# Kernel tuning notes

Hardware: AMD Instinct MI355X
Metric: run time of the kernel (lower is better)

Reference implementation:

```python
import jax, jax.numpy as jnp
import numpy as np

MOMENTUM = 0.999
TEMP = 0.07
NUM_HARD_NEGS = 16
NUM_CLASSES = 20000


def _normalize(x, axis=-1, eps=1e-12):
    n = jnp.linalg.norm(x, axis=axis, keepdims=True)
    return x / jnp.maximum(n, eps)


def setup_inputs() -> dict:
    key = jax.random.key(0)
    k1, k2, k3, k4, k5 = jax.random.split(key, 5)
    B, K, Dp, De, C = 512, 8, 256, 512, NUM_CLASSES
    return {
        "part_features": jax.random.normal(k1, (B, K, Dp), dtype=jnp.float32),
        "embeddings": jax.random.normal(k2, (B, De), dtype=jnp.float32),
        "sat_emb": jax.random.normal(k3, (B, De), dtype=jnp.float32),
        "part_bank": jax.random.normal(k4, (C, K, Dp), dtype=jnp.float32) * 0.01,
        "embed_bank": jax.random.normal(k5, (C, De), dtype=jnp.float32) * 0.01,
        "labels": jnp.arange(B, dtype=jnp.int64),
    }


def reference(part_features, embeddings, sat_emb, part_bank, embed_bank, labels):
    m = MOMENTUM
    B = embeddings.shape[0]
    C = embed_bank.shape[0]

    # --- EMA scatter update (bank assumed initialized for all classes) ---
    # labels are distinct, so vectorized scatter == sequential python loop.
    new_part_bank = part_bank.at[labels].set(
        m * part_bank[labels] + (1.0 - m) * part_features)
    new_embed_bank = embed_bank.at[labels].set(
        m * embed_bank[labels] + (1.0 - m) * embeddings)

    # Banks are torch buffers updated under no_grad -> stop_gradient.
    eb = jax.lax.stop_gradient(new_embed_bank)

    # --- PrototypeNCE ---
    q = _normalize(embeddings)                      # [B, De]
    protos = _normalize(eb)                         # [C, De]
    sim = (q @ protos.T) / TEMP                     # [B, C]
    pos_sim = jnp.take_along_axis(sim, labels[:, None], axis=1)  # [B, 1]
    class_ids = jnp.arange(C)
    pos_mask = labels[:, None] == class_ids[None, :]
    neg_sim = jnp.where(pos_mask, -1e9, sim)
    hard_negs, _ = jax.lax.top_k(neg_sim, NUM_HARD_NEGS)          # [B, k]
    logits = jnp.concatenate([pos_sim, hard_negs], axis=1)       # [B, 1+k]
    nce_loss = jnp.mean(jax.nn.logsumexp(logits, axis=1) - logits[:, 0])

    # --- Cross-view prototype alignment ---
    p = _normalize(eb[labels])                      # [B, De]
    d = _normalize(embeddings)
    s = _normalize(sat_emb)
    align_loss = 0.5 * (jnp.mean(1.0 - jnp.sum(d * p, axis=-1))
                        + jnp.mean(1.0 - jnp.sum(s * p, axis=-1)))

    return new_part_bank, new_embed_bank, nce_loss, align_loss
```

## Files before the change

kernel.cpp:

```cpp
#include <hip/hip_runtime.h>
#include <math.h>

#define MOM 0.999f
#define ONE_M_MOM 0.001f
#define INV_TEMP (1.0f / 0.07f)
#define C_CLASSES 20000
#define B_SZ 512
#define DE 512
#define PART_ROW 2048
#define PART_BANK_N (C_CLASSES * PART_ROW)
#define EMB_BANK_N (C_CLASSES * DE)
#define NEG_INF (-3.0e38f)
#define NTILE 157
#define NGEMM (4 * NTILE)
#define NCHUNK 2500
#define NPARTB 512

typedef __attribute__((ext_vector_type(8))) short short8;
typedef __attribute__((ext_vector_type(4))) float f32x4;

__device__ inline unsigned short f2bf_rne(float f) {
    unsigned u = __builtin_bit_cast(unsigned, f);
    return (unsigned short)((u + 0x7FFFu + ((u >> 16) & 1u)) >> 16);
}

__device__ inline float bf2f(unsigned short u) {
    return __builtin_bit_cast(float, (unsigned)u << 16);
}

__device__ inline void gload16(const void* g, void* l) {
    __builtin_amdgcn_global_load_lds(
        (const __attribute__((address_space(1))) unsigned int*)g,
        (__attribute__((address_space(3))) unsigned int*)l, 16, 0, 0);
}

__global__ void embed_qnorm(const float* __restrict__ ebank, const float* __restrict__ emb,
                            const int* __restrict__ labels, float* __restrict__ out_eb,
                            unsigned short* __restrict__ Bb, float* __restrict__ inv_norm,
                            unsigned short* __restrict__ Ab, int* __restrict__ counter) {
    int w = threadIdx.x >> 6, l = threadIdx.x & 63;
    int blk = blockIdx.x;
    if (blk == 0 && threadIdx.x == 0) *counter = 0;
    if (blk < 5000) {
        int c = blk * 4 + w;
        int m = -1;
#pragma unroll
        for (int k = 0; k < 8; ++k)
            if (labels[l + k * 64] == c) m = l + k * 64;
#pragma unroll
        for (int off = 32; off; off >>= 1) m = max(m, __shfl_xor(m, off));

        const float4* row = (const float4*)(ebank + ((long)c << 9));
        float4 v0 = row[2 * l], v1 = row[2 * l + 1];
        if (m >= 0) {
            const float4* nr = (const float4*)(emb + ((long)m << 9));
            float4 n0 = nr[2 * l], n1 = nr[2 * l + 1];
            v0.x = MOM * v0.x + ONE_M_MOM * n0.x;
            v0.y = MOM * v0.y + ONE_M_MOM * n0.y;
            v0.z = MOM * v0.z + ONE_M_MOM * n0.z;
            v0.w = MOM * v0.w + ONE_M_MOM * n0.w;
            v1.x = MOM * v1.x + ONE_M_MOM * n1.x;
            v1.y = MOM * v1.y + ONE_M_MOM * n1.y;
            v1.z = MOM * v1.z + ONE_M_MOM * n1.z;
            v1.w = MOM * v1.w + ONE_M_MOM * n1.w;
        }
        float4* orow = (float4*)(out_eb + ((long)c << 9));
        orow[2 * l] = v0; orow[2 * l + 1] = v1;
        float ss = v0.x * v0.x + v0.y * v0.y + v0.z * v0.z + v0.w * v0.w
                 + v1.x * v1.x + v1.y * v1.y + v1.z * v1.z + v1.w * v1.w;
#pragma unroll
        for (int off = 32; off; off >>= 1) ss += __shfl_xor(ss, off);
        if (l == 0) inv_norm[c] = 1.0f / fmaxf(sqrtf(ss), 1e-12f);
        short8 o;
        o[0] = (short)f2bf_rne(v0.x); o[1] = (short)f2bf_rne(v0.y);
        o[2] = (short)f2bf_rne(v0.z); o[3] = (short)f2bf_rne(v0.w);
        o[4] = (short)f2bf_rne(v1.x); o[5] = (short)f2bf_rne(v1.y);
        o[6] = (short)f2bf_rne(v1.z); o[7] = (short)f2bf_rne(v1.w);
        *(short8*)(Bb + ((long)c << 9) + l * 8) = o;
    } else {
        int b = (blk - 5000) * 4 + w;
        const float4* row = (const float4*)(emb + ((long)b << 9));
        float4 v0 = row[2 * l], v1 = row[2 * l + 1];
        float ss = v0.x * v0.x + v0.y * v0.y + v0.z * v0.z + v0.w * v0.w
                 + v1.x * v1.x + v1.y * v1.y + v1.z * v1.z + v1.w * v1.w;
#pragma unroll
        for (int off = 32; off; off >>= 1) ss += __shfl_xor(ss, off);
        float inv = 1.0f / fmaxf(sqrtf(ss), 1e-12f);
        v0.x *= inv; v0.y *= inv; v0.z *= inv; v0.w *= inv;
        v1.x *= inv; v1.y *= inv; v1.z *= inv; v1.w *= inv;
        short8 o;
        o[0] = (short)f2bf_rne(v0.x); o[1] = (short)f2bf_rne(v0.y);
        o[2] = (short)f2bf_rne(v0.z); o[3] = (short)f2bf_rne(v0.w);
        o[4] = (short)f2bf_rne(v1.x); o[5] = (short)f2bf_rne(v1.y);
        o[6] = (short)f2bf_rne(v1.z); o[7] = (short)f2bf_rne(v1.w);
        *(short8*)(Ab + ((long)b << 9) + l * 8) = o;
    }
}

__global__ void __launch_bounds__(256)
part_gemm(const unsigned short* __restrict__ A, const unsigned short* __restrict__ B,
          const float* __restrict__ inv_norm, const int* __restrict__ labels,
          float* __restrict__ partials,
          const float4* __restrict__ pb, const float4* __restrict__ pf,
          float4* __restrict__ out_pb) {
    __shared__ unsigned short smem[128 * 130];

    if (blockIdx.x >= NGEMM) {
        int t = threadIdx.x;
        int* mbs = (int*)smem;
        int la = labels[t], lb = labels[t + 256];
        for (int chunk = blockIdx.x - NGEMM; chunk < NCHUNK; chunk += NPARTB) {
            int c0 = chunk * 8;
            __syncthreads();
            if (t < 8) mbs[t] = -1;
            __syncthreads();
#pragma unroll
            for (int r = 0; r < 8; ++r) {
                if (la == c0 + r) mbs[r] = t;
                if (lb == c0 + r) mbs[r] = t + 256;
            }
            __syncthreads();
            const float4* src = pb + (long)c0 * (PART_ROW / 4);
            float4* dst = out_pb + (long)c0 * (PART_ROW / 4);
            float4 v[16];
#pragma unroll
            for (int i = 0; i < 16; ++i) v[i] = src[t + i * 256];
#pragma unroll
            for (int i = 0; i < 16; ++i) {
                int mb = mbs[i >> 1];
                if (mb >= 0) {
                    float4 n = pf[(long)mb * (PART_ROW / 4) + (t + (i & 1) * 256)];
                    v[i].x = MOM * v[i].x + ONE_M_MOM * n.x;
                    v[i].y = MOM * v[i].y + ONE_M_MOM * n.y;
                    v[i].z = MOM * v[i].z + ONE_M_MOM * n.z;
                    v[i].w = MOM * v[i].w + ONE_M_MOM * n.w;
                }
                dst[t + i * 256] = v[i];
            }
        }
        return;
    }

    unsigned short* Asm = smem;
    unsigned short* Bsm = smem + 8192;

    const int t = threadIdx.x;
    const int w = t >> 6, l = t & 63;
    const int wr = w >> 1, wc = w & 1;

    int id = blockIdx.x;
    int xcd = id & 7, idx = id >> 3;
    int wg = (xcd < 4) ? xcd * 79 + idx : 316 + (xcd - 4) * 78 + idx;
    const int bm = wg & 3, bn = wg >> 2;

    f32x4 acc[4][4] = {};

    const int srow = t >> 3;
    const long swz = ((t & 7) ^ (srow & 7)) << 3;
    const unsigned short* Ag = A + ((long)(bm * 128 + srow) << 9) + swz;
    const unsigned short* Bg[4];
#pragma unroll
    for (int i = 0; i < 4; ++i) {
        int br = bn * 128 + i * 32 + srow;
        if (br > C_CLASSES - 1) br = C_CLASSES - 1;
        Bg[i] = B + ((long)br << 9) + swz;
    }
    char* Adst = (char*)Asm + (w << 10);
    char* Bdst = (char*)Bsm + (w << 10);

    const int fr = l & 15;
    const int s4 = l >> 4;
    const int swr0 = ((s4) ^ (fr & 7)) << 4;
    const int swr1 = ((4 + s4) ^ (fr & 7)) << 4;

    for (int kt = 0; kt < 8; ++kt) {
        const int ko = kt << 6;
#pragma unroll
        for (int i = 0; i < 4; ++i) {
            gload16(Ag + ko + ((long)i << 14), Adst + (i << 12));
            gload16(Bg[i] + ko, Bdst + (i << 12));
        }
        __syncthreads();
        short8 af[2][4], bf[2][4];
        const char* Abase = (const char*)Asm;
        const char* Bbase = (const char*)Bsm;
#pragma unroll
        for (int m = 0; m < 4; ++m) {
            int ra = (wr * 64 + m * 16 + fr) << 7;
            int rb = (wc * 64 + m * 16 + fr) << 7;
            af[0][m] = *(const short8*)(Abase + ra + swr0);
            af[1][m] = *(const short8*)(Abase + ra + swr1);
            bf[0][m] = *(const short8*)(Bbase + rb + swr0);
            bf[1][m] = *(const short8*)(Bbase + rb + swr1);
        }
        __builtin_amdgcn_s_setprio(1);
#pragma unroll
        for (int kk = 0; kk < 2; ++kk)
#pragma unroll
            for (int m = 0; m < 4; ++m)
#pragma unroll
                for (int n = 0; n < 4; ++n)
                    acc[m][n] = __builtin_amdgcn_mfma_f32_16x16x32_bf16(
                        af[kk][m], bf[kk][n], acc[m][n], 0, 0, 0);
        __builtin_amdgcn_s_setprio(0);
        __syncthreads();
    }

    unsigned short* stile = smem;
    const int r4 = s4 << 2;
#pragma unroll
    for (int n = 0; n < 4; ++n) {
        int ct = wc * 64 + fr + n * 16;
        int cg = bn * 128 + ct;
        bool ok = cg < C_CLASSES;
        float sc = ok ? inv_norm[cg] * INV_TEMP : 0.0f;
#pragma unroll
        for (int m = 0; m < 4; ++m) {
            int rt = wr * 64 + r4 + m * 16;
#pragma unroll
            for (int j = 0; j < 4; ++j) {
                float v = ok ? acc[m][n][j] * sc : NEG_INF;
                stile[(rt + j) * 130 + ct] = f2bf_rne(v);
            }
        }
    }
    __syncthreads();

    const int r = t >> 1, half = t & 1;
    const int gr = bm * 128 + r;
    const int lab = labels[gr];
    const int lab_l = lab - (bn << 7) - (half << 6);
    const unsigned short* bp = stile + r * 130 + half * 64;
    float tl[16];
#pragma unroll
    for (int j = 0; j < 16; ++j) tl[j] = NEG_INF;
    for (int c = 0; c < 64; ++c) {
        if (c == lab_l) continue;
        float v = bf2f(bp[c]);
        if (v > tl[15]) {
            tl[15] = v;
#pragma unroll
            for (int j = 15; j > 0; --j) {
                float a = tl[j - 1], bb = tl[j];
                if (bb > a) { tl[j - 1] = bb; tl[j] = a; }
            }
        }
    }
    float ol[16];
#pragma unroll
    for (int j = 0; j < 16; ++j) ol[j] = __shfl_xor(tl[j], 1);
    if (half == 0) {
        float4 o0, o1, o2, o3;
        o0.x = fmaxf(tl[0],  ol[15]); o0.y = fmaxf(tl[1],  ol[14]);
        o0.z = fmaxf(tl[2],  ol[13]); o0.w = fmaxf(tl[3],  ol[12]);
        o1.x = fmaxf(tl[4],  ol[11]); o1.y = fmaxf(tl[5],  ol[10]);
        o1.z = fmaxf(tl[6],  ol[9]);  o1.w = fmaxf(tl[7],  ol[8]);
        o2.x = fmaxf(tl[8],  ol[7]);  o2.y = fmaxf(tl[9],  ol[6]);
        o2.z = fmaxf(tl[10], ol[5]);  o2.w = fmaxf(tl[11], ol[4]);
        o3.x = fmaxf(tl[12], ol[3]);  o3.y = fmaxf(tl[13], ol[2]);
        o3.z = fmaxf(tl[14], ol[1]);  o3.w = fmaxf(tl[15], ol[0]);
        float4* op4 = (float4*)(partials + ((long)gr * NTILE + bn) * 16);
        op4[0] = o0; op4[1] = o1; op4[2] = o2; op4[3] = o3;
    }
}

__global__ void __launch_bounds__(64)
merge_fin(const float* __restrict__ partials, const float* __restrict__ emb,
          const float* __restrict__ out_eb, const float* __restrict__ sat,
          const float* __restrict__ inv_norm, const int* __restrict__ labels,
          float* __restrict__ lnce, float* __restrict__ lalign,
          int* __restrict__ counter, float* __restrict__ out_losses) {
    int b = blockIdx.x;
    int l = threadIdx.x;
    const float4* pr4 = (const float4*)(partials + (long)b * (NTILE * 16));

    float tl[16];
#pragma unroll
    for (int j = 0; j < 16; ++j) tl[j] = NEG_INF;
    for (int i = l; i < NTILE * 4; i += 64) {
        float4 v4 = pr4[i];
        float vv[4] = {v4.x, v4.y, v4.z, v4.w};
#pragma unroll
        for (int q = 0; q < 4; ++q) {
            float v = vv[q];
            if (v > tl[15]) {
                tl[15] = v;
#pragma unroll
                for (int j = 15; j > 0; --j) {
                    float a = tl[j - 1], bb = tl[j];
                    if (bb > a) { tl[j - 1] = bb; tl[j] = a; }
                }
            }
        }
    }

    float M = 0.f, S = 0.f;
#pragma unroll 1
    for (int j = 0; j < 16; ++j) {
        float v = tl[0];
        float mx = v;
#pragma unroll
        for (int off = 32; off; off >>= 1) mx = fmaxf(mx, __shfl_xor(mx, off));
        unsigned long long ball = __ballot(v == mx);
        int win = (int)(__ffsll((unsigned long long)ball)) - 1;
        if (l == win) {
#pragma unroll
            for (int q = 0; q < 15; ++q) tl[q] = tl[q + 1];
            tl[15] = NEG_INF;
        }
        if (j == 0) { M = mx; S = 1.0f; }
        else S += expf(mx - M);
    }

    int lab = labels[b];
    const float4* qr = (const float4*)(emb + ((long)b << 9));
    const float4* er = (const float4*)(out_eb + ((long)lab << 9));
    const float4* sr = (const float4*)(sat + ((long)b << 9));
    float a1 = 0.f, a2 = 0.f, a3 = 0.f, a4 = 0.f;
#pragma unroll
    for (int rr = 0; rr < 2; ++rr) {
        int j = 2 * l + rr;
        float4 d4 = qr[j], s4 = sr[j], e4 = er[j];
        a1 += d4.x * e4.x + d4.y * e4.y + d4.z * e4.z + d4.w * e4.w;
        a2 += s4.x * e4.x + s4.y * e4.y + s4.z * e4.z + s4.w * e4.w;
        a3 += s4.x * s4.x + s4.y * s4.y + s4.z * s4.z + s4.w * s4.w;
        a4 += d4.x * d4.x + d4.y * d4.y + d4.z * d4.z + d4.w * d4.w;
    }
#pragma unroll
    for (int off = 32; off; off >>= 1) {
        a1 += __shfl_xor(a1, off);
        a2 += __shfl_xor(a2, off);
        a3 += __shfl_xor(a3, off);
        a4 += __shfl_xor(a4, off);
    }
    int done = 0;
    if (l == 0) {
        float invl = inv_norm[lab];
        float invq = 1.0f / fmaxf(sqrtf(a4), 1e-12f);
        float pos = a1 * invq * invl * INV_TEMP;
        float mx2 = fmaxf(M, pos);
        float ssum = expf(M - mx2) * S + expf(pos - mx2);
        lnce[b] = logf(ssum) + mx2 - pos;
        float pd = a1 * invq * invl;
        float ps = a2 * invl / fmaxf(sqrtf(a3), 1e-12f);
        lalign[b] = 1.0f - 0.5f * (pd + ps);
        __threadfence();
        done = (atomicAdd(counter, 1) == B_SZ - 1) ? 1 : 0;
    }
    done = __shfl(done, 0);
    if (done) {
        __threadfence();
        volatile const float* vn = lnce;
        volatile const float* va = lalign;
        float s1 = 0.f, s2 = 0.f;
#pragma unroll
        for (int k = 0; k < B_SZ / 64; ++k) {
            s1 += vn[l + k * 64];
            s2 += va[l + k * 64];
        }
#pragma unroll
        for (int off = 32; off; off >>= 1) {
            s1 += __shfl_xor(s1, off);
            s2 += __shfl_xor(s2, off);
        }
        if (l == 0) {
            out_losses[0] = s1 / (float)B_SZ;
            out_losses[1] = s2 / (float)B_SZ;
            *counter = 0;
        }
    }
}

extern "C" void kernel_launch(void* const* d_in, const int* in_sizes, int n_in,
                              void* d_out, int out_size, void* d_ws, size_t ws_size,
                              hipStream_t stream) {
    const float* pf = (const float*)d_in[0];
    const float* emb = (const float*)d_in[1];
    const float* sat = (const float*)d_in[2];
    const float* pb = (const float*)d_in[3];
    const float* ebank = (const float*)d_in[4];
    const int* labels = (const int*)d_in[5];

    float* out = (float*)d_out;
    float* out_pb = out;
    float* out_eb = out + PART_BANK_N;
    float* out_losses = out + PART_BANK_N + EMB_BANK_N;

    float* ws = (float*)d_ws;
    float* inv_norm = ws;
    int* counter = (int*)(inv_norm + C_CLASSES);
    float* lnce = (float*)(counter + 16);
    float* lalign = lnce + B_SZ;
    float* partials = lalign + B_SZ;
    unsigned short* Ab = (unsigned short*)(partials + (long)B_SZ * NTILE * 16);
    unsigned short* Bb = Ab + (long)B_SZ * DE;

    embed_qnorm<<<5000 + 128, 256, 0, stream>>>(ebank, emb, labels, out_eb, Bb, inv_norm,
                                                Ab, counter);
    part_gemm<<<NGEMM + NPARTB, 256, 0, stream>>>(Ab, Bb, inv_norm, labels, partials,
                                                  (const float4*)pb, (const float4*)pf,
                                                  (float4*)out_pb);
    merge_fin<<<B_SZ, 64, 0, stream>>>(partials, emb, out_eb, sat, inv_norm,
                                       labels, lnce, lalign, counter, out_losses);
}
```

Before: 157.1 us.

## Move part-bank EMA streaming from GEMM kernel into the embed-normalize kernel

Moves the part_bank EMA copy out of the GEMM kernel and into the first elementwise kernel, giving each 8-class chunk its own block instead of 512 persistent looping blocks. The GEMM+top-k kernel now launches only its tile blocks. This removes contention between the bandwidth-heavy copy and the GEMM tiles and drops the extra syncthreads per loop iteration. In exchange, the copy no longer overlaps with GEMM compute and becomes serialized before it.

```diff
diff --git a/kernel.cpp b/kernel.cpp
--- a/kernel.cpp
+++ b/kernel.cpp
@@ -14,7 +14,6 @@
 #define NTILE 157
 #define NGEMM (4 * NTILE)
 #define NCHUNK 2500
-#define NPARTB 512
 
 typedef __attribute__((ext_vector_type(8))) short short8;
 typedef __attribute__((ext_vector_type(4))) float f32x4;
@@ -34,15 +33,52 @@
         (__attribute__((address_space(3))) unsigned int*)l, 16, 0, 0);
 }
 
-__global__ void embed_qnorm(const float* __restrict__ ebank, const float* __restrict__ emb,
-                            const int* __restrict__ labels, float* __restrict__ out_eb,
-                            unsigned short* __restrict__ Bb, float* __restrict__ inv_norm,
-                            unsigned short* __restrict__ Ab, int* __restrict__ counter) {
-    int w = threadIdx.x >> 6, l = threadIdx.x & 63;
+__global__ void __launch_bounds__(256)
+stream_all(const float4* __restrict__ pf4, const float* __restrict__ emb,
+           const int* __restrict__ labels, const float4* __restrict__ pb,
+           const float* __restrict__ ebank, float4* __restrict__ out_pb,
+           float* __restrict__ out_eb, unsigned short* __restrict__ Bb,
+           float* __restrict__ inv_norm, unsigned short* __restrict__ Ab,
+           int* __restrict__ counter) {
     int blk = blockIdx.x;
-    if (blk == 0 && threadIdx.x == 0) *counter = 0;
-    if (blk < 5000) {
-        int c = blk * 4 + w;
+    int t = threadIdx.x;
+    if (blk == 0 && t == 0) *counter = 0;
+
+    if (blk < NCHUNK) {
+        __shared__ int mbs[8];
+        int c0 = blk * 8;
+        if (t < 8) mbs[t] = -1;
+        __syncthreads();
+        int la = labels[t], lb = labels[t + 256];
+#pragma unroll
+        for (int r = 0; r < 8; ++r) {
+            if (la == c0 + r) mbs[r] = t;
+            if (lb == c0 + r) mbs[r] = t + 256;
+        }
+        __syncthreads();
+        const float4* src = pb + (long)c0 * (PART_ROW / 4);
+        float4* dst = out_pb + (long)c0 * (PART_ROW / 4);
+        float4 v[16];
+#pragma unroll
+        for (int i = 0; i < 16; ++i) v[i] = src[t + i * 256];
+#pragma unroll
+        for (int i = 0; i < 16; ++i) {
+            int mb = mbs[i >> 1];
+            if (mb >= 0) {
+                float4 n = pf4[(long)mb * (PART_ROW / 4) + (t + (i & 1) * 256)];
+                v[i].x = MOM * v[i].x + ONE_M_MOM * n.x;
+                v[i].y = MOM * v[i].y + ONE_M_MOM * n.y;
+                v[i].z = MOM * v[i].z + ONE_M_MOM * n.z;
+                v[i].w = MOM * v[i].w + ONE_M_MOM * n.w;
+            }
+            dst[t + i * 256] = v[i];
+        }
+        return;
+    }
+
+    int w = t >> 6, l = t & 63;
+    if (blk < NCHUNK + 5000) {
+        int c = (blk - NCHUNK) * 4 + w;
         int m = -1;
 #pragma unroll
         for (int k = 0; k < 8; ++k)
@@ -78,7 +114,7 @@
         o[6] = (short)f2bf_rne(v1.z); o[7] = (short)f2bf_rne(v1.w);
         *(short8*)(Bb + ((long)c << 9) + l * 8) = o;
     } else {
-        int b = (blk - 5000) * 4 + w;
+        int b = (blk - NCHUNK - 5000) * 4 + w;
         const float4* row = (const float4*)(emb + ((long)b << 9));
         float4 v0 = row[2 * l], v1 = row[2 * l + 1];
         float ss = v0.x * v0.x + v0.y * v0.y + v0.z * v0.z + v0.w * v0.w
@@ -98,49 +134,10 @@
 }
 
 __global__ void __launch_bounds__(256)
-part_gemm(const unsigned short* __restrict__ A, const unsigned short* __restrict__ B,
+gemm_topk(const unsigned short* __restrict__ A, const unsigned short* __restrict__ B,
           const float* __restrict__ inv_norm, const int* __restrict__ labels,
-          float* __restrict__ partials,
-          const float4* __restrict__ pb, const float4* __restrict__ pf,
-          float4* __restrict__ out_pb) {
+          float* __restrict__ partials) {
     __shared__ unsigned short smem[128 * 130];
-
-    if (blockIdx.x >= NGEMM) {
-        int t = threadIdx.x;
-        int* mbs = (int*)smem;
-        int la = labels[t], lb = labels[t + 256];
-        for (int chunk = blockIdx.x - NGEMM; chunk < NCHUNK; chunk += NPARTB) {
-            int c0 = chunk * 8;
-            __syncthreads();
-            if (t < 8) mbs[t] = -1;
-            __syncthreads();
-#pragma unroll
-            for (int r = 0; r < 8; ++r) {
-                if (la == c0 + r) mbs[r] = t;
-                if (lb == c0 + r) mbs[r] = t + 256;
-            }
-            __syncthreads();
-            const float4* src = pb + (long)c0 * (PART_ROW / 4);
-            float4* dst = out_pb + (long)c0 * (PART_ROW / 4);
-            float4 v[16];
-#pragma unroll
-            for (int i = 0; i < 16; ++i) v[i] = src[t + i * 256];
-#pragma unroll
-            for (int i = 0; i < 16; ++i) {
-                int mb = mbs[i >> 1];
-                if (mb >= 0) {
-                    float4 n = pf[(long)mb * (PART_ROW / 4) + (t + (i & 1) * 256)];
-                    v[i].x = MOM * v[i].x + ONE_M_MOM * n.x;
-                    v[i].y = MOM * v[i].y + ONE_M_MOM * n.y;
-                    v[i].z = MOM * v[i].z + ONE_M_MOM * n.z;
-                    v[i].w = MOM * v[i].w + ONE_M_MOM * n.w;
-                }
-                dst[t + i * 256] = v[i];
-            }
-        }
-        return;
-    }
-
     unsigned short* Asm = smem;
     unsigned short* Bsm = smem + 8192;
 
@@ -395,11 +392,10 @@
     unsigned short* Ab = (unsigned short*)(partials + (long)B_SZ * NTILE * 16);
     unsigned short* Bb = Ab + (long)B_SZ * DE;
 
-    embed_qnorm<<<5000 + 128, 256, 0, stream>>>(ebank, emb, labels, out_eb, Bb, inv_norm,
-                                                Ab, counter);
-    part_gemm<<<NGEMM + NPARTB, 256, 0, stream>>>(Ab, Bb, inv_norm, labels, partials,
-                                                  (const float4*)pb, (const float4*)pf,
-                                                  (float4*)out_pb);
+    stream_all<<<NCHUNK + 5000 + 128, 256, 0, stream>>>(
+        (const float4*)pf, emb, labels, (const float4*)pb, ebank,
+        (float4*)out_pb, out_eb, Bb, inv_norm, Ab, counter);
+    gemm_topk<<<NGEMM, 256, 0, stream>>>(Ab, Bb, inv_norm, labels, partials);
     merge_fin<<<B_SZ, 64, 0, stream>>>(partials, emb, out_eb, sat, inv_norm,
                                        labels, lnce, lalign, counter, out_losses);
 }
```

Result: slower. 175.7 us (+11.8%).
